# Optimization experiments

Measured on AMD Instinct MI355X. Metric: run time of the kernel, lower is better.

## Reference

```python
import jax, jax.numpy as jnp
import numpy as np


def rotate_half(x):
    d = x.shape[-1] // 2
    return jnp.concatenate([-x[..., d:], x[..., :d]], axis=-1)


def setup_inputs() -> dict:
    key = jax.random.key(0)
    ks = jax.random.split(key, 8)
    B, T, C, H = 2, 2048, 2048, 16
    hd = C // H
    x = jax.random.normal(ks[0], (B, T, C), dtype=jnp.float32)
    # realistic RoPE tables
    inv_freq = 1.0 / (10000.0 ** (jnp.arange(0, hd, 2, dtype=jnp.float32) / hd))
    t = jnp.arange(T, dtype=jnp.float32)
    freqs = jnp.einsum('t,f->tf', t, inv_freq)
    emb = jnp.concatenate([freqs, freqs], axis=-1)  # [T, hd]
    cos = jnp.cos(emb)
    sin = jnp.sin(emb)
    mask = jnp.tril(jnp.ones((T, T), dtype=bool))[None, None]  # causal [1,1,T,T]
    s = C ** -0.5
    Wq = jax.random.normal(ks[1], (C, C), dtype=jnp.float32) * s
    Wk = jax.random.normal(ks[2], (C, C), dtype=jnp.float32) * s
    Wv = jax.random.normal(ks[3], (C, C), dtype=jnp.float32) * s
    Wo = jax.random.normal(ks[4], (C, C), dtype=jnp.float32) * s
    return {"x": x, "cos": cos, "sin": sin, "mask": mask,
            "Wq": Wq, "Wk": Wk, "Wv": Wv, "Wo": Wo}


def reference(x, cos, sin, mask, Wq, Wk, Wv, Wo):
    B, T, C = x.shape
    H = 16
    hd = C // H
    scale = hd ** -0.5
    # projections: torch Linear stores W as [out,in], y = x @ W^T
    def proj(W):
        return jnp.einsum('btc,dc->btd', x, W).reshape(B, T, H, hd).transpose(0, 2, 1, 3)
    q, k, v = proj(Wq), proj(Wk), proj(Wv)  # [B,H,T,hd]
    c = cos[None, None]  # [1,1,T,hd]
    s = sin[None, None]
    q = q * c + rotate_half(q) * s
    k = k * c + rotate_half(k) * s
    attn = jnp.einsum('bhqd,bhkd->bhqk', q, k) * scale
    attn = jnp.where(mask, attn, -jnp.inf)
    attn = jax.nn.softmax(attn, axis=-1)
    out = jnp.einsum('bhqk,bhkd->bhqd', attn, v)
    out = out.transpose(0, 2, 1, 3).reshape(B, T, C)
    return jnp.einsum('btc,dc->btd', out, Wo)
```

## Files before the change

### kernel.cpp

```cpp
#include <hip/hip_runtime.h>
#include <cstdint>

typedef __bf16 bf16_t;
typedef __bf16 bf16x8 __attribute__((ext_vector_type(8)));
typedef __bf16 bf16x4 __attribute__((ext_vector_type(4)));
typedef float  f32x4  __attribute__((ext_vector_type(4)));

#define BB 2
#define TT 2048
#define CC 2048
#define HH 16
#define HD 128

static __device__ __forceinline__ void async_copy16(const void* gp, void* lp) {
  __builtin_amdgcn_global_load_lds(
      (const __attribute__((address_space(1))) void*)(uintptr_t)gp,
      (__attribute__((address_space(3))) void*)(uint32_t)(uintptr_t)lp,
      16, 0, 0);
}

__global__ __launch_bounds__(256)
void cast_all(const float* __restrict__ x, const float* __restrict__ wq,
              const float* __restrict__ wk, const float* __restrict__ wv,
              const float* __restrict__ wo, bf16_t* __restrict__ xb,
              bf16_t* __restrict__ wq_b) {
  const int NX4 = (BB * TT * CC) / 4;
  const int NW4 = (CC * CC) / 4;
  int i = blockIdx.x * 256 + threadIdx.x;
  const float* s;
  bf16_t* d;
  int off;
  if (i < NX4) {
    s = x; d = xb; off = i;
  } else {
    int j = i - NX4;
    int w = j >> 20;
    off = j & (NW4 - 1);
    s = (w == 0) ? wq : (w == 1) ? wk : (w == 2) ? wv : wo;
    d = wq_b + (size_t)w * (CC * CC);
  }
  float4 v = ((const float4*)s)[off];
  bf16x4 o;
  o[0] = (bf16_t)v.x; o[1] = (bf16_t)v.y; o[2] = (bf16_t)v.z; o[3] = (bf16_t)v.w;
  ((bf16x4*)d)[off] = o;
}

__global__ __launch_bounds__(256)
void gemm_v(const bf16_t* __restrict__ A, const bf16_t* __restrict__ Bw,
            bf16_t* __restrict__ C2, int Kdim) {
  __shared__ __align__(16) char smem[128 * 136 * 2];
  bf16_t* As = (bf16_t*)smem;
  bf16_t* Bs = (bf16_t*)(smem + 16384);
  const int tid  = threadIdx.x;
  const int wave = tid >> 6, lane = tid & 63;
  const int quad = lane >> 4, l16 = lane & 15;
  const int m0 = blockIdx.y * 128, n0 = blockIdx.x * 128;
  const int wm = (wave >> 1) * 64, wn = (wave & 1) * 64;

  f32x4 acc[4][4] = {};

  const int srow = lane >> 3;
  const int scol = (((lane & 7) ^ srow) & 7) * 8;
  const int swz  = (l16 & 7) * 8;

  for (int k0 = 0; k0 < Kdim; k0 += 64) {
#pragma unroll
    for (int i = 0; i < 4; ++i) {
      int chunk = wave * 4 + i;
      int row = chunk * 8 + srow;
      async_copy16(A + (size_t)(m0 + row) * Kdim + k0 + scol, As + chunk * 512);
    }
#pragma unroll
    for (int i = 0; i < 4; ++i) {
      int chunk = wave * 4 + i;
      int row = chunk * 8 + srow;
      async_copy16(Bw + (size_t)(n0 + row) * Kdim + k0 + scol, Bs + chunk * 512);
    }
    __syncthreads();
#pragma unroll
    for (int kk = 0; kk < 64; kk += 32) {
      const int koff = (kk + quad * 8) ^ swz;
      bf16x8 af[4], bfr[4];
#pragma unroll
      for (int i = 0; i < 4; ++i)
        af[i] = *(const bf16x8*)&As[(wm + i * 16 + l16) * 64 + koff];
#pragma unroll
      for (int j = 0; j < 4; ++j)
        bfr[j] = *(const bf16x8*)&Bs[(wn + j * 16 + l16) * 64 + koff];
#pragma unroll
      for (int i = 0; i < 4; ++i)
#pragma unroll
        for (int j = 0; j < 4; ++j)
          acc[i][j] = __builtin_amdgcn_mfma_f32_16x16x32_bf16(af[i], bfr[j], acc[i][j], 0, 0, 0);
    }
    __syncthreads();
  }

  const int h = (n0 & (CC - 1)) >> 7;
  bf16_t* Ct = (bf16_t*)smem;
  __syncthreads();
#pragma unroll
  for (int i = 0; i < 4; ++i)
#pragma unroll
    for (int j = 0; j < 4; ++j) {
      int c = wn + j * 16 + l16;
#pragma unroll
      for (int r = 0; r < 4; ++r)
        Ct[(wm + i * 16 + quad * 4 + r) * 136 + c] = (bf16_t)acc[i][j][r];
    }
  __syncthreads();
  const unsigned short* Cu = (const unsigned short*)Ct;
  int col = tid >> 1;
  int rh  = (tid & 1) * 64;
  int grow0 = m0 + rh;
  int b = grow0 >> 11, t0 = grow0 & (TT - 1);
  unsigned int pk[32];
#pragma unroll
  for (int s = 0; s < 32; ++s) {
    unsigned int lo = Cu[(rh + 2 * s) * 136 + col];
    unsigned int hi = Cu[(rh + 2 * s + 1) * 136 + col];
    pk[s] = lo | (hi << 16);
  }
  bf16_t* dstp = C2 + ((size_t)(b * HH + h) * HD + col) * TT + t0;
#pragma unroll
  for (int u = 0; u < 8; ++u) {
    uint4 w; w.x = pk[4*u]; w.y = pk[4*u+1]; w.z = pk[4*u+2]; w.w = pk[4*u+3];
    *(uint4*)(dstp + 8 * u) = w;
  }
}

__global__ __launch_bounds__(512, 2)
void gemm_qkv256(const bf16_t* __restrict__ A, const bf16_t* __restrict__ Bw,
                 bf16_t* __restrict__ Qo, bf16_t* __restrict__ Ko,
                 const float* __restrict__ cosT, const float* __restrict__ sinT,
                 int Kdim) {
  extern __shared__ __align__(16) char smem[];
  bf16_t* lds = (bf16_t*)smem;
  const int tid  = threadIdx.x;
  const int wave = tid >> 6, lane = tid & 63;
  const int quad = lane >> 4, l16 = lane & 15;
  const int wm = wave >> 2, wn = wave & 3;
  const int n0 = blockIdx.x * 256, m0 = blockIdx.y * 256;

  const int srow = lane >> 3;
  const int scol = ((lane & 7) ^ srow) * 8;
  const int swz  = (l16 & 7) * 8;
  const int nK = Kdim >> 6;

  const bf16_t* Ag = A  + (size_t)(m0 + wave * 32 + srow) * Kdim + scol;
  const bf16_t* Bg = Bw + (size_t)(n0 + wave * 32 + srow) * Kdim + scol;
  const int ldsChunk = wave * 4 * 512;

#define STAGE_A(kt, buf)                                                      \
  {                                                                           \
    bf16_t* dstA = lds + (buf) * 32768 + ldsChunk;                            \
    const bf16_t* srcA = Ag + (kt) * 64;                                      \
    _Pragma("unroll")                                                         \
    for (int ci = 0; ci < 4; ++ci)                                            \
      async_copy16(srcA + (size_t)(ci * 8) * Kdim, dstA + ci * 512);          \
  }
#define STAGE_B(kt, buf)                                                      \
  {                                                                           \
    bf16_t* dstB = lds + (buf) * 32768 + 16384 + ldsChunk;                    \
    const bf16_t* srcB = Bg + (kt) * 64;                                      \
    _Pragma("unroll")                                                         \
    for (int ci = 0; ci < 4; ++ci)                                            \
      async_copy16(srcB + (size_t)(ci * 8) * Kdim, dstB + ci * 512);          \
  }

  f32x4 acc[8][4] = {};
  STAGE_A(0, 0); STAGE_B(0, 0); STAGE_A(1, 1); STAGE_B(1, 1);

  const int k0off = (quad * 8) ^ swz;
  const int k1off = (32 + quad * 8) ^ swz;

  for (int k = 0; k < nK; ++k) {
    const int cur = k & 1;
    const bf16_t* Asb = lds + cur * 32768;
    const bf16_t* Bsb = Asb + 16384;
    if (k < nK - 1) asm volatile("s_waitcnt vmcnt(8)" ::: "memory");
    else            asm volatile("s_waitcnt vmcnt(0)" ::: "memory");
    __builtin_amdgcn_s_barrier();
    __builtin_amdgcn_sched_barrier(0);

    bf16x8 a0[8], b0[4], a1[8], b1[4];
#pragma unroll
    for (int i = 0; i < 8; ++i)
      a0[i] = *(const bf16x8*)&Asb[(wm * 128 + i * 16 + l16) * 64 + k0off];
#pragma unroll
    for (int j = 0; j < 4; ++j)
      b0[j] = *(const bf16x8*)&Bsb[(wn * 64 + j * 16 + l16) * 64 + k0off];
    asm volatile("s_waitcnt lgkmcnt(0)" ::: "memory");
    __builtin_amdgcn_sched_barrier(0);
    __builtin_amdgcn_s_setprio(1);
#pragma unroll
    for (int i = 0; i < 4; ++i)
#pragma unroll
      for (int j = 0; j < 4; ++j)
        acc[i][j] = __builtin_amdgcn_mfma_f32_16x16x32_bf16(a0[i], b0[j], acc[i][j], 0, 0, 0);
    __builtin_amdgcn_s_setprio(0);

#pragma unroll
    for (int i = 0; i < 8; ++i)
      a1[i] = *(const bf16x8*)&Asb[(wm * 128 + i * 16 + l16) * 64 + k1off];
#pragma unroll
    for (int j = 0; j < 4; ++j)
      b1[j] = *(const bf16x8*)&Bsb[(wn * 64 + j * 16 + l16) * 64 + k1off];
    __builtin_amdgcn_s_setprio(1);
#pragma unroll
    for (int i = 4; i < 8; ++i)
#pragma unroll
      for (int j = 0; j < 4; ++j)
        acc[i][j] = __builtin_amdgcn_mfma_f32_16x16x32_bf16(a0[i], b0[j], acc[i][j], 0, 0, 0);
    __builtin_amdgcn_s_setprio(0);
    asm volatile("s_waitcnt lgkmcnt(0)" ::: "memory");
    __builtin_amdgcn_s_barrier();
    __builtin_amdgcn_sched_barrier(0);

    if (k + 2 < nK) STAGE_A(k + 2, cur);
    __builtin_amdgcn_s_setprio(1);
#pragma unroll
    for (int i = 0; i < 4; ++i)
#pragma unroll
      for (int j = 0; j < 4; ++j)
        acc[i][j] = __builtin_amdgcn_mfma_f32_16x16x32_bf16(a1[i], b1[j], acc[i][j], 0, 0, 0);
    __builtin_amdgcn_s_setprio(0);

    if (k + 2 < nK) STAGE_B(k + 2, cur);
    __builtin_amdgcn_s_setprio(1);
#pragma unroll
    for (int i = 4; i < 8; ++i)
#pragma unroll
      for (int j = 0; j < 4; ++j)
        acc[i][j] = __builtin_amdgcn_mfma_f32_16x16x32_bf16(a1[i], b1[j], acc[i][j], 0, 0, 0);
    __builtin_amdgcn_s_setprio(0);
  }
#undef STAGE_A
#undef STAGE_B

  {
    const int proj = n0 >> 11;
    bf16_t* dst = proj == 0 ? Qo : Ko;
    bf16_t* Ct = lds;
#pragma unroll
    for (int i = 0; i < 8; ++i)
#pragma unroll
      for (int j = 0; j < 4; ++j) {
        int coll = wn * 64 + j * 16 + l16;
        int pcol = coll + ((coll >> 7) << 2);
#pragma unroll
        for (int r = 0; r < 4; ++r) {
          int rowl = wm * 128 + i * 16 + quad * 4 + r;
          Ct[rowl * 268 + pcol] = (bf16_t)acc[i][j][r];
        }
      }
    __syncthreads();
    const int lane16 = tid & 15;
    const int slot0  = tid >> 4;
    const int d0 = lane16 * 8;
    const int dp = d0 ^ 64;
    const float sgn = (d0 < 64) ? -1.f : 1.f;
    const int b = m0 >> 11;
    const int hbase = (n0 & (CC - 1)) >> 7;
#pragma unroll
    for (int p = 0; p < 16; ++p) {
      int gslot = p * 32 + slot0;
      int rowl = gslot >> 1, hh = gslot & 1;
      int t = (m0 + rowl) & (TT - 1);
      const bf16_t* src = Ct + rowl * 268 + hh * 132;
      bf16x8 self = *(const bf16x8*)(src + d0);
      bf16x8 part = *(const bf16x8*)(src + dp);
      const float* ct = cosT + t * HD + d0;
      const float* st = sinT + t * HD + d0;
      float4 c0 = *(const float4*)(ct);
      float4 c1 = *(const float4*)(ct + 4);
      float4 s0 = *(const float4*)(st);
      float4 s1 = *(const float4*)(st + 4);
      float cc[8] = {c0.x, c0.y, c0.z, c0.w, c1.x, c1.y, c1.z, c1.w};
      float ss[8] = {s0.x, s0.y, s0.z, s0.w, s1.x, s1.y, s1.z, s1.w};
      bf16x8 o8;
#pragma unroll
      for (int e = 0; e < 8; ++e)
        o8[e] = (bf16_t)((float)self[e] * cc[e] + sgn * (float)part[e] * ss[e]);
      *(bf16x8*)(dst + (((size_t)(b * HH + hbase + hh) * TT + t) * HD) + d0) = o8;
    }
  }
}

__global__ __launch_bounds__(512, 2)
void gemm_wo(const bf16_t* __restrict__ A, const bf16_t* __restrict__ Bw,
             float* __restrict__ C, int Kdim) {
  extern __shared__ __align__(16) char smem[];
  bf16_t* lds = (bf16_t*)smem;
  const int tid  = threadIdx.x;
  const int wave = tid >> 6, lane = tid & 63;
  const int quad = lane >> 4, l16 = lane & 15;
  const int wm = wave >> 2, wn = wave & 3;
  const int n0 = blockIdx.x * 256, m0 = blockIdx.y * 128;

  const int srow = lane >> 3;
  const int scol = ((lane & 7) ^ srow) * 8;
  const int swz  = (l16 & 7) * 8;
  const int nK = Kdim >> 6;

#define WSTAGE_A(kt, buf)                                                     \
  {                                                                           \
    bf16_t* d_ = lds + (buf) * 24576;                                         \
    _Pragma("unroll")                                                         \
    for (int c_ = 0; c_ < 2; ++c_) {                                          \
      int ch_ = wave * 2 + c_;                                                \
      async_copy16(A + (size_t)(m0 + ch_ * 8 + srow) * Kdim + (kt) * 64 + scol,\
                   d_ + ch_ * 512);                                           \
    }                                                                         \
  }
#define WSTAGE_B(kt, buf)                                                     \
  {                                                                           \
    bf16_t* d_ = lds + (buf) * 24576 + 8192;                                  \
    _Pragma("unroll")                                                         \
    for (int c_ = 0; c_ < 4; ++c_) {                                          \
      int ch_ = wave * 4 + c_;                                                \
      async_copy16(Bw + (size_t)(n0 + ch_ * 8 + srow) * Kdim + (kt) * 64 + scol,\
                   d_ + ch_ * 512);                                           \
    }                                                                         \
  }

  f32x4 acc[4][4] = {};
  WSTAGE_A(0, 0); WSTAGE_B(0, 0); WSTAGE_A(1, 1); WSTAGE_B(1, 1);

  const int k0off = (quad * 8) ^ swz;
  const int k1off = (32 + quad * 8) ^ swz;

  for (int k = 0; k < nK; ++k) {
    const int cur = k & 1;
    const bf16_t* As = lds + cur * 24576;
    const bf16_t* Bs = As + 8192;
    if (k < nK - 1) asm volatile("s_waitcnt vmcnt(6)" ::: "memory");
    else            asm volatile("s_waitcnt vmcnt(0)" ::: "memory");
    __builtin_amdgcn_s_barrier();
    __builtin_amdgcn_sched_barrier(0);

    bf16x8 a0[4], b0[4], a1[4], b1[4];
#pragma unroll
    for (int i = 0; i < 4; ++i)
      a0[i] = *(const bf16x8*)&As[(wm * 64 + i * 16 + l16) * 64 + k0off];
#pragma unroll
    for (int j = 0; j < 4; ++j)
      b0[j] = *(const bf16x8*)&Bs[(wn * 64 + j * 16 + l16) * 64 + k0off];
    asm volatile("s_waitcnt lgkmcnt(0)" ::: "memory");
    __builtin_amdgcn_sched_barrier(0);
    __builtin_amdgcn_s_setprio(1);
#pragma unroll
    for (int i = 0; i < 4; ++i)
#pragma unroll
      for (int j = 0; j < 2; ++j)
        acc[i][j] = __builtin_amdgcn_mfma_f32_16x16x32_bf16(a0[i], b0[j], acc[i][j], 0, 0, 0);
    __builtin_amdgcn_s_setprio(0);

#pragma unroll
    for (int i = 0; i < 4; ++i)
      a1[i] = *(const bf16x8*)&As[(wm * 64 + i * 16 + l16) * 64 + k1off];
#pragma unroll
    for (int j = 0; j < 4; ++j)
      b1[j] = *(const bf16x8*)&Bs[(wn * 64 + j * 16 + l16) * 64 + k1off];
    __builtin_amdgcn_s_setprio(1);
#pragma unroll
    for (int i = 0; i < 4; ++i)
#pragma unroll
      for (int j = 2; j < 4; ++j)
        acc[i][j] = __builtin_amdgcn_mfma_f32_16x16x32_bf16(a0[i], b0[j], acc[i][j], 0, 0, 0);
    __builtin_amdgcn_s_setprio(0);
    asm volatile("s_waitcnt lgkmcnt(0)" ::: "memory");
    __builtin_amdgcn_s_barrier();
    __builtin_amdgcn_sched_barrier(0);

    if (k + 2 < nK) WSTAGE_A(k + 2, cur);
    __builtin_amdgcn_s_setprio(1);
#pragma unroll
    for (int i = 0; i < 4; ++i)
#pragma unroll
      for (int j = 0; j < 2; ++j)
        acc[i][j] = __builtin_amdgcn_mfma_f32_16x16x32_bf16(a1[i], b1[j], acc[i][j], 0, 0, 0);
    __builtin_amdgcn_s_setprio(0);

    if (k + 2 < nK) WSTAGE_B(k + 2, cur);
    __builtin_amdgcn_s_setprio(1);
#pragma unroll
    for (int i = 0; i < 4; ++i)
#pragma unroll
      for (int j = 2; j < 4; ++j)
        acc[i][j] = __builtin_amdgcn_mfma_f32_16x16x32_bf16(a1[i], b1[j], acc[i][j], 0, 0, 0);
    __builtin_amdgcn_s_setprio(0);
  }
#undef WSTAGE_A
#undef WSTAGE_B

#pragma unroll
  for (int i = 0; i < 4; ++i)
#pragma unroll
    for (int j = 0; j < 4; ++j) {
      int gcol = n0 + wn * 64 + j * 16 + l16;
#pragma unroll
      for (int r = 0; r < 4; ++r) {
        int grow = m0 + wm * 64 + i * 16 + quad * 4 + r;
        C[(size_t)grow * CC + gcol] = acc[i][j][r];
      }
    }
}

__global__ __launch_bounds__(256, 2)
void attn_kernel(const bf16_t* __restrict__ Q, const bf16_t* __restrict__ K,
                 const bf16_t* __restrict__ Vt, bf16_t* __restrict__ Out) {
  __shared__ __align__(16) bf16_t Ks[2][64 * 128];
  __shared__ __align__(16) bf16_t Vs[2][128 * 64];
  __shared__ __align__(16) bf16_t Pl[4][16 * 64];
  const int lane = threadIdx.x & 63, wave = threadIdx.x >> 6;
  const int quad = lane >> 4, l16 = lane & 15;
  const int linear = blockIdx.x;
  const int hb = linear & 31;
  const int h = hb & (HH - 1), b = hb >> 4;
  const int qt = (TT / 128 - 1) - (linear >> 5);
  const int q0 = qt * 128 + wave * 32;
  const size_t qkbase = (size_t)(b * HH + h) * TT * HD;
  const bf16_t* Kh = K + qkbase;
  const bf16_t* Vh = Vt + (size_t)(b * HH + h) * HD * TT;
  const float scale = 0.08838834764831845f;

  const int srK = lane >> 4;
  const int sgK = lane & 15;
  const int scK0 = (sgK ^ srK) * 8;
  const int scK1 = (sgK ^ (4 + srK)) * 8;
  const int srV = lane >> 3;
  const int scV = (((lane & 7) ^ srV) & 7) * 8;
  const int swz = (l16 & 7) * 8;
  const int psw = (l16 & 7) << 3;

  bf16x8 qf[2][4];
#pragma unroll
  for (int mt = 0; mt < 2; ++mt) {
    const bf16_t* qrow = Q + qkbase + (size_t)(q0 + mt * 16 + l16) * HD;
#pragma unroll
    for (int kc = 0; kc < 4; ++kc) qf[mt][kc] = *(const bf16x8*)(qrow + kc * 32 + quad * 8);
  }

  f32x4 o[2][8] = {};
  float l_i[2][4] = {};

  const int nIter = qt * 2 + 2;

  {
#pragma unroll
    for (int i = 0; i < 4; ++i) {
      int chunk = wave * 4 + i;
      int sc = (chunk & 1) ? scK1 : scK0;
      async_copy16(Kh + (size_t)(chunk * 4 + srK) * HD + sc, &Ks[0][chunk * 512]);
    }
#pragma unroll
    for (int i = 0; i < 4; ++i) {
      int chunk = wave * 4 + i;
      async_copy16(Vh + (size_t)(chunk * 8 + srV) * TT + scV, &Vs[0][chunk * 512]);
    }
  }

  for (int it = 0; it < nIter; ++it) {
    const int cur = it & 1;
    const int key0 = it * 64;
    __syncthreads();

    if (it + 1 < nIter) {
      const int nxt = cur ^ 1;
      const int knxt = key0 + 64;
#pragma unroll
      for (int i = 0; i < 4; ++i) {
        int chunk = wave * 4 + i;
        int sc = (chunk & 1) ? scK1 : scK0;
        async_copy16(Kh + (size_t)(knxt + chunk * 4 + srK) * HD + sc, &Ks[nxt][chunk * 512]);
      }
#pragma unroll
      for (int i = 0; i < 4; ++i) {
        int chunk = wave * 4 + i;
        async_copy16(Vh + (size_t)(chunk * 8 + srV) * TT + knxt + scV, &Vs[nxt][chunk * 512]);
      }
    }

    f32x4 s[2][4] = {};
#pragma unroll
    for (int kc = 0; kc < 4; ++kc) {
      const int koff = (kc * 32 + quad * 8) ^ swz;
#pragma unroll
      for (int kt = 0; kt < 4; ++kt) {
        bf16x8 kf = *(const bf16x8*)&Ks[cur][(kt * 16 + l16) * 128 + koff];
        s[0][kt] = __builtin_amdgcn_mfma_f32_16x16x32_bf16(qf[0][kc], kf, s[0][kt], 0, 0, 0);
        s[1][kt] = __builtin_amdgcn_mfma_f32_16x16x32_bf16(qf[1][kc], kf, s[1][kt], 0, 0, 0);
      }
    }

    bf16_t* pl = &Pl[wave][0];
    bf16x8 pf[2][2];
#pragma unroll
    for (int mt = 0; mt < 2; ++mt) {
#pragma unroll
      for (int r = 0; r < 4; ++r) {
        int prow = quad * 4 + r;
        int rel = q0 + mt * 16 + prow - key0;
        int rbase = prow * 64;
        int sw = (prow & 7) << 3;
        float lr = 0.f;
#pragma unroll
        for (int kt = 0; kt < 4; ++kt) {
          int c16 = kt * 16 + l16;
          float e = (c16 > rel) ? 0.f : __expf(s[mt][kt][r] * scale);
          lr += e;
          pl[rbase + (c16 ^ sw)] = (bf16_t)e;
        }
        l_i[mt][r] += lr;
      }
      pf[mt][0] = *(const bf16x8*)&pl[l16 * 64 + ((quad * 8) ^ psw)];
      pf[mt][1] = *(const bf16x8*)&pl[l16 * 64 + ((32 + quad * 8) ^ psw)];
      __builtin_amdgcn_sched_barrier(0);
    }

    const int voff0 = (quad * 8) ^ swz;
    const int voff1 = (32 + quad * 8) ^ swz;
#pragma unroll
    for (int n = 0; n < 8; ++n) {
      bf16x8 vf0 = *(const bf16x8*)&Vs[cur][(n * 16 + l16) * 64 + voff0];
      bf16x8 vf1 = *(const bf16x8*)&Vs[cur][(n * 16 + l16) * 64 + voff1];
      o[0][n] = __builtin_amdgcn_mfma_f32_16x16x32_bf16(pf[0][0], vf0, o[0][n], 0, 0, 0);
      o[0][n] = __builtin_amdgcn_mfma_f32_16x16x32_bf16(pf[0][1], vf1, o[0][n], 0, 0, 0);
      o[1][n] = __builtin_amdgcn_mfma_f32_16x16x32_bf16(pf[1][0], vf0, o[1][n], 0, 0, 0);
      o[1][n] = __builtin_amdgcn_mfma_f32_16x16x32_bf16(pf[1][1], vf1, o[1][n], 0, 0, 0);
    }
  }

#pragma unroll
  for (int mt = 0; mt < 2; ++mt)
#pragma unroll
    for (int r = 0; r < 4; ++r) {
      float l = l_i[mt][r];
#pragma unroll
      for (int off = 1; off < 16; off <<= 1) l += __shfl_xor(l, off);
      l_i[mt][r] = 1.f / l;
    }

#pragma unroll
  for (int mt = 0; mt < 2; ++mt)
#pragma unroll
    for (int n = 0; n < 8; ++n)
#pragma unroll
      for (int r = 0; r < 4; ++r) {
        int qg = q0 + mt * 16 + quad * 4 + r;
        size_t off = ((size_t)(b * TT + qg) * CC) + h * HD + n * 16 + l16;
        Out[off] = (bf16_t)(o[mt][n][r] * l_i[mt][r]);
      }
}

extern "C" void kernel_launch(void* const* d_in, const int* in_sizes, int n_in,
                              void* d_out, int out_size, void* d_ws, size_t ws_size,
                              hipStream_t stream) {
  const float* x    = (const float*)d_in[0];
  const float* cosT = (const float*)d_in[1];
  const float* sinT = (const float*)d_in[2];
  const float* Wq = (const float*)d_in[4];
  const float* Wk = (const float*)d_in[5];
  const float* Wv = (const float*)d_in[6];
  const float* Wo = (const float*)d_in[7];
  float* out = (float*)d_out;

  char* ws = (char*)d_ws;
  const size_t XSZ = (size_t)BB * TT * CC * 2;
  const size_t WSZ = (size_t)CC * CC * 2;
  bf16_t* x_bf  = (bf16_t*)(ws);
  bf16_t* wq_bf = (bf16_t*)(ws + XSZ);
  bf16_t* wv_bf = (bf16_t*)(ws + XSZ + 2 * WSZ);
  bf16_t* wo_bf = (bf16_t*)(ws + XSZ + 3 * WSZ);
  bf16_t* Qb    = (bf16_t*)(ws + XSZ + 4 * WSZ);
  bf16_t* Kb    = (bf16_t*)(ws + 2 * XSZ + 4 * WSZ);
  bf16_t* Vt    = (bf16_t*)(ws + 3 * XSZ + 4 * WSZ);
  bf16_t* attn_bf = x_bf;

  const int NX = BB * TT * CC;
  const int NW = CC * CC;
  cast_all<<<(NX / 4 + 4 * (NW / 4)) / 256, 256, 0, stream>>>(
      x, Wq, Wk, Wv, Wo, x_bf, wq_bf);

  (void)hipFuncSetAttribute(reinterpret_cast<const void*>(gemm_qkv256),
                            hipFuncAttributeMaxDynamicSharedMemorySize, 137216);
  gemm_qkv256<<<dim3(2 * CC / 256, BB * TT / 256), 512, 137216, stream>>>(
      x_bf, wq_bf, Qb, Kb, cosT, sinT, CC);

  gemm_v<<<dim3(CC / 128, BB * TT / 128), 256, 0, stream>>>(
      x_bf, wv_bf, Vt, CC);

  attn_kernel<<<dim3(BB * HH * (TT / 128)), 256, 0, stream>>>(Qb, Kb, Vt, attn_bf);

  (void)hipFuncSetAttribute(reinterpret_cast<const void*>(gemm_wo),
                            hipFuncAttributeMaxDynamicSharedMemorySize, 98304);
  gemm_wo<<<dim3(CC / 256, BB * TT / 128), 512, 98304, stream>>>(
      attn_bf, wo_bf, out, CC);
}
```

Measured before the change: 367.1 us.

## Pair causal query tiles per block and use 8 waves of 16 rows

The attention kernel now launches 256 blocks of 512 threads, and each block processes two query tiles in sequence (tile 15-s, then tile s). This balances causal work so every block does the same number of key iterations. Each wave now owns 16 query rows instead of 32, so K/V tiles in shared memory are reused by 8 waves and each wave's MFMA work per tile halves. The trade-off is fewer independent MFMA chains per wave, lower per-wave arithmetic intensity on LDS reads, and only 256 blocks to fill the GPU.

```diff
diff --git a/kernel.cpp b/kernel.cpp
--- a/kernel.cpp
+++ b/kernel.cpp
@@ -407,19 +407,18 @@
     }
 }
 
-__global__ __launch_bounds__(256, 2)
+__global__ __launch_bounds__(512, 2)
 void attn_kernel(const bf16_t* __restrict__ Q, const bf16_t* __restrict__ K,
                  const bf16_t* __restrict__ Vt, bf16_t* __restrict__ Out) {
   __shared__ __align__(16) bf16_t Ks[2][64 * 128];
   __shared__ __align__(16) bf16_t Vs[2][128 * 64];
-  __shared__ __align__(16) bf16_t Pl[4][16 * 64];
+  __shared__ __align__(16) bf16_t Pl[8][16 * 64];
   const int lane = threadIdx.x & 63, wave = threadIdx.x >> 6;
   const int quad = lane >> 4, l16 = lane & 15;
   const int linear = blockIdx.x;
   const int hb = linear & 31;
   const int h = hb & (HH - 1), b = hb >> 4;
-  const int qt = (TT / 128 - 1) - (linear >> 5);
-  const int q0 = qt * 128 + wave * 32;
+  const int spair = linear >> 5;
   const size_t qkbase = (size_t)(b * HH + h) * TT * HD;
   const bf16_t* Kh = K + qkbase;
   const bf16_t* Vh = Vt + (size_t)(b * HH + h) * HD * TT;
@@ -434,124 +433,118 @@
   const int swz = (l16 & 7) * 8;
   const int psw = (l16 & 7) << 3;
 
-  bf16x8 qf[2][4];
-#pragma unroll
-  for (int mt = 0; mt < 2; ++mt) {
-    const bf16_t* qrow = Q + qkbase + (size_t)(q0 + mt * 16 + l16) * HD;
-#pragma unroll
-    for (int kc = 0; kc < 4; ++kc) qf[mt][kc] = *(const bf16x8*)(qrow + kc * 32 + quad * 8);
-  }
-
-  f32x4 o[2][8] = {};
-  float l_i[2][4] = {};
-
-  const int nIter = qt * 2 + 2;
-
-  {
-#pragma unroll
-    for (int i = 0; i < 4; ++i) {
-      int chunk = wave * 4 + i;
-      int sc = (chunk & 1) ? scK1 : scK0;
-      async_copy16(Kh + (size_t)(chunk * 4 + srK) * HD + sc, &Ks[0][chunk * 512]);
-    }
-#pragma unroll
-    for (int i = 0; i < 4; ++i) {
-      int chunk = wave * 4 + i;
-      async_copy16(Vh + (size_t)(chunk * 8 + srV) * TT + scV, &Vs[0][chunk * 512]);
-    }
-  }
-
-  for (int it = 0; it < nIter; ++it) {
-    const int cur = it & 1;
-    const int key0 = it * 64;
-    __syncthreads();
-
-    if (it + 1 < nIter) {
-      const int nxt = cur ^ 1;
-      const int knxt = key0 + 64;
-#pragma unroll
-      for (int i = 0; i < 4; ++i) {
-        int chunk = wave * 4 + i;
+#pragma unroll
+  for (int half = 0; half < 2; ++half) {
+    const int qt = half == 0 ? (15 - spair) : spair;
+    const int q0 = qt * 128 + wave * 16;
+    const int nIter = qt * 2 + 2;
+
+    bf16x8 qf[4];
+    {
+      const bf16_t* qrow = Q + qkbase + (size_t)(q0 + l16) * HD;
+#pragma unroll
+      for (int kc = 0; kc < 4; ++kc) qf[kc] = *(const bf16x8*)(qrow + kc * 32 + quad * 8);
+    }
+
+    f32x4 o[8] = {};
+    float l_i[4] = {};
+
+    {
+#pragma unroll
+      for (int i = 0; i < 2; ++i) {
+        int chunk = wave * 2 + i;
         int sc = (chunk & 1) ? scK1 : scK0;
-        async_copy16(Kh + (size_t)(knxt + chunk * 4 + srK) * HD + sc, &Ks[nxt][chunk * 512]);
-      }
-#pragma unroll
-      for (int i = 0; i < 4; ++i) {
-        int chunk = wave * 4 + i;
-        async_copy16(Vh + (size_t)(chunk * 8 + srV) * TT + knxt + scV, &Vs[nxt][chunk * 512]);
-      }
-    }
-
-    f32x4 s[2][4] = {};
-#pragma unroll
-    for (int kc = 0; kc < 4; ++kc) {
-      const int koff = (kc * 32 + quad * 8) ^ swz;
-#pragma unroll
-      for (int kt = 0; kt < 4; ++kt) {
-        bf16x8 kf = *(const bf16x8*)&Ks[cur][(kt * 16 + l16) * 128 + koff];
-        s[0][kt] = __builtin_amdgcn_mfma_f32_16x16x32_bf16(qf[0][kc], kf, s[0][kt], 0, 0, 0);
-        s[1][kt] = __builtin_amdgcn_mfma_f32_16x16x32_bf16(qf[1][kc], kf, s[1][kt], 0, 0, 0);
-      }
-    }
-
-    bf16_t* pl = &Pl[wave][0];
-    bf16x8 pf[2][2];
-#pragma unroll
-    for (int mt = 0; mt < 2; ++mt) {
+        async_copy16(Kh + (size_t)(chunk * 4 + srK) * HD + sc, &Ks[0][chunk * 512]);
+      }
+#pragma unroll
+      for (int i = 0; i < 2; ++i) {
+        int chunk = wave * 2 + i;
+        async_copy16(Vh + (size_t)(chunk * 8 + srV) * TT + scV, &Vs[0][chunk * 512]);
+      }
+    }
+
+    for (int it = 0; it < nIter; ++it) {
+      const int cur = it & 1;
+      const int key0 = it * 64;
+      __syncthreads();
+
+      if (it + 1 < nIter) {
+        const int nxt = cur ^ 1;
+        const int knxt = key0 + 64;
+#pragma unroll
+        for (int i = 0; i < 2; ++i) {
+          int chunk = wave * 2 + i;
+          int sc = (chunk & 1) ? scK1 : scK0;
+          async_copy16(Kh + (size_t)(knxt + chunk * 4 + srK) * HD + sc, &Ks[nxt][chunk * 512]);
+        }
+#pragma unroll
+        for (int i = 0; i < 2; ++i) {
+          int chunk = wave * 2 + i;
+          async_copy16(Vh + (size_t)(chunk * 8 + srV) * TT + knxt + scV, &Vs[nxt][chunk * 512]);
+        }
+      }
+
+      f32x4 s[4] = {};
+#pragma unroll
+      for (int kc = 0; kc < 4; ++kc) {
+        const int koff = (kc * 32 + quad * 8) ^ swz;
+#pragma unroll
+        for (int kt = 0; kt < 4; ++kt) {
+          bf16x8 kf = *(const bf16x8*)&Ks[cur][(kt * 16 + l16) * 128 + koff];
+          s[kt] = __builtin_amdgcn_mfma_f32_16x16x32_bf16(qf[kc], kf, s[kt], 0, 0, 0);
+        }
+      }
+
+      {
+        bf16_t* pl = &Pl[wave][0];
+#pragma unroll
+        for (int r = 0; r < 4; ++r) {
+          int prow = quad * 4 + r;
+          int rel = q0 + prow - key0;
+          int rbase = prow * 64;
+          int sw = (prow & 7) << 3;
+          float lr = 0.f;
+#pragma unroll
+          for (int kt = 0; kt < 4; ++kt) {
+            int c16 = kt * 16 + l16;
+            float e = (c16 > rel) ? 0.f : __expf(s[kt][r] * scale);
+            lr += e;
+            pl[rbase + (c16 ^ sw)] = (bf16_t)e;
+          }
+          l_i[r] += lr;
+        }
+      }
+
+      bf16x8 pf0 = *(const bf16x8*)&Pl[wave][l16 * 64 + ((quad * 8) ^ psw)];
+      bf16x8 pf1 = *(const bf16x8*)&Pl[wave][l16 * 64 + ((32 + quad * 8) ^ psw)];
+      const int voff0 = (quad * 8) ^ swz;
+      const int voff1 = (32 + quad * 8) ^ swz;
+#pragma unroll
+      for (int n = 0; n < 8; ++n) {
+        bf16x8 vf0 = *(const bf16x8*)&Vs[cur][(n * 16 + l16) * 64 + voff0];
+        bf16x8 vf1 = *(const bf16x8*)&Vs[cur][(n * 16 + l16) * 64 + voff1];
+        o[n] = __builtin_amdgcn_mfma_f32_16x16x32_bf16(pf0, vf0, o[n], 0, 0, 0);
+        o[n] = __builtin_amdgcn_mfma_f32_16x16x32_bf16(pf1, vf1, o[n], 0, 0, 0);
+      }
+    }
+
+#pragma unroll
+    for (int r = 0; r < 4; ++r) {
+      float l = l_i[r];
+#pragma unroll
+      for (int off = 1; off < 16; off <<= 1) l += __shfl_xor(l, off);
+      l_i[r] = 1.f / l;
+    }
+
+#pragma unroll
+    for (int n = 0; n < 8; ++n)
 #pragma unroll
       for (int r = 0; r < 4; ++r) {
-        int prow = quad * 4 + r;
-        int rel = q0 + mt * 16 + prow - key0;
-        int rbase = prow * 64;
-        int sw = (prow & 7) << 3;
-        float lr = 0.f;
-#pragma unroll
-        for (int kt = 0; kt < 4; ++kt) {
-          int c16 = kt * 16 + l16;
-          float e = (c16 > rel) ? 0.f : __expf(s[mt][kt][r] * scale);
-          lr += e;
-          pl[rbase + (c16 ^ sw)] = (bf16_t)e;
-        }
-        l_i[mt][r] += lr;
-      }
-      pf[mt][0] = *(const bf16x8*)&pl[l16 * 64 + ((quad * 8) ^ psw)];
-      pf[mt][1] = *(const bf16x8*)&pl[l16 * 64 + ((32 + quad * 8) ^ psw)];
-      __builtin_amdgcn_sched_barrier(0);
-    }
-
-    const int voff0 = (quad * 8) ^ swz;
-    const int voff1 = (32 + quad * 8) ^ swz;
-#pragma unroll
-    for (int n = 0; n < 8; ++n) {
-      bf16x8 vf0 = *(const bf16x8*)&Vs[cur][(n * 16 + l16) * 64 + voff0];
-      bf16x8 vf1 = *(const bf16x8*)&Vs[cur][(n * 16 + l16) * 64 + voff1];
-      o[0][n] = __builtin_amdgcn_mfma_f32_16x16x32_bf16(pf[0][0], vf0, o[0][n], 0, 0, 0);
-      o[0][n] = __builtin_amdgcn_mfma_f32_16x16x32_bf16(pf[0][1], vf1, o[0][n], 0, 0, 0);
-      o[1][n] = __builtin_amdgcn_mfma_f32_16x16x32_bf16(pf[1][0], vf0, o[1][n], 0, 0, 0);
-      o[1][n] = __builtin_amdgcn_mfma_f32_16x16x32_bf16(pf[1][1], vf1, o[1][n], 0, 0, 0);
-    }
-  }
-
-#pragma unroll
-  for (int mt = 0; mt < 2; ++mt)
-#pragma unroll
-    for (int r = 0; r < 4; ++r) {
-      float l = l_i[mt][r];
-#pragma unroll
-      for (int off = 1; off < 16; off <<= 1) l += __shfl_xor(l, off);
-      l_i[mt][r] = 1.f / l;
-    }
-
-#pragma unroll
-  for (int mt = 0; mt < 2; ++mt)
-#pragma unroll
-    for (int n = 0; n < 8; ++n)
-#pragma unroll
-      for (int r = 0; r < 4; ++r) {
-        int qg = q0 + mt * 16 + quad * 4 + r;
+        int qg = q0 + quad * 4 + r;
         size_t off = ((size_t)(b * TT + qg) * CC) + h * HD + n * 16 + l16;
-        Out[off] = (bf16_t)(o[mt][n][r] * l_i[mt][r]);
-      }
+        Out[off] = (bf16_t)(o[n][r] * l_i[r]);
+      }
+  }
 }
 
 extern "C" void kernel_launch(void* const* d_in, const int* in_sizes, int n_in,
@@ -591,7 +584,7 @@
   gemm_v<<<dim3(CC / 128, BB * TT / 128), 256, 0, stream>>>(
       x_bf, wv_bf, Vt, CC);
 
-  attn_kernel<<<dim3(BB * HH * (TT / 128)), 256, 0, stream>>>(Qb, Kb, Vt, attn_bf);
+  attn_kernel<<<dim3(BB * HH * 8), 512, 0, stream>>>(Qb, Kb, Vt, attn_bf);
 
   (void)hipFuncSetAttribute(reinterpret_cast<const void*>(gemm_wo),
                             hipFuncAttributeMaxDynamicSharedMemorySize, 98304);
```

Result: faster. 351.9 us (-4.1%).
